# Optimization experiments

Hardware: AMD Instinct MI355X
Metric: run time of the kernel (lower is better)

## Reference

```python
import jax, jax.numpy as jnp
import numpy as np

B, N, C, H, D, K = 4, 8192, 384, 12, 2, 256
M = N // K          # 32 members per cluster
CH = C // H         # 32 head dim


def setup_inputs() -> dict:
    key = jax.random.key(0)
    ks = jax.random.split(key, 8)
    pos = jax.random.uniform(ks[0], (B, N, D), jnp.float32) * 100.0
    feat = jax.random.normal(ks[1], (B, N, C), jnp.float32)
    # each batch's points partitioned into K clusters of M members (a permutation)
    perms = jax.vmap(lambda kk: jax.random.permutation(kk, N))(jax.random.split(ks[2], B))
    member_idx = perms.reshape(B * K, M).astype(jnp.int32)               # z x m
    batch_idx = jnp.broadcast_to(
        jnp.repeat(jnp.arange(B, dtype=jnp.int32), K)[:, None], (B * K, M))
    w = 0.02
    qkv_w = jax.random.normal(ks[3], (3 * C, C), jnp.float32) * w
    qkv_b = jnp.zeros((3 * C,), jnp.float32)
    pos_w = jax.random.normal(ks[4], (H, D), jnp.float32) * w
    pos_b = jnp.zeros((H,), jnp.float32)
    proj_w = jax.random.normal(ks[5], (C, C), jnp.float32) * w
    proj_b = jnp.zeros((C,), jnp.float32)
    return dict(pos=pos, feat=feat, member_idx=member_idx, batch_idx=batch_idx,
                qkv_w=qkv_w, qkv_b=qkv_b, pos_w=pos_w, pos_b=pos_b,
                proj_w=proj_w, proj_b=proj_b, k=K)


def reference(pos, feat, member_idx, batch_idx, qkv_w, qkv_b, pos_w, pos_b,
              proj_w, proj_b, k):
    # attend_means=True, mask=None, cluster_score=None, q_subsample_idx=None path
    b, n, c = feat.shape
    d = pos.shape[2]
    h = pos_w.shape[0]
    ch = c // h
    z, m = member_idx.shape
    scale = ch ** -0.5

    qkv = feat @ qkv_w.T + qkv_b            # b,n,3c
    q = qkv[..., :c]                        # b,n,c
    kv = qkv[..., c:]                       # b,n,2c

    pos_orig = pos
    pos_n = pos / jnp.max(pos.reshape(-1, d), axis=0)   # per-coordinate max norm

    # irregular gather of kv / pos per cluster member
    kv_g = kv[batch_idx, member_idx]        # z,m,2c
    pos_g = pos_n[batch_idx, member_idx]    # z,m,d

    # cluster_score=None, mask=None -> uniform weights 1/m (mean over members)
    kv_mean = jnp.mean(kv_g, axis=1).reshape(b, k, 2, h, ch)
    pos_mean = jnp.mean(pos_g, axis=1).reshape(b, k, d)

    key_ = kv_mean[:, :, 0].transpose(0, 2, 1, 3)   # b,h,k,ch
    v = kv_mean[:, :, 1].transpose(0, 2, 1, 3)      # b,h,k,ch
    qh = q.reshape(b, n, h, ch).transpose(0, 2, 1, 3) * scale  # b,h,n,ch

    attn = jnp.einsum('bhnc,bhkc->bhnk', qh, key_)  # b,h,n,k
    rel_pos = pos_mean[:, None, :, :] - pos_orig[:, :, None, :]  # b,n,k,d
    pos_bias = jnp.einsum('bnkd,hd->bhnk', rel_pos, pos_w) + pos_b[None, :, None, None]
    attn = jax.nn.softmax(attn + pos_bias, axis=-1)

    out = jnp.einsum('bhnk,bhkc->bnhc', attn, v).reshape(b, n, c)
    return out @ proj_w.T + proj_b
```

## Files before the change

### kernel.cpp

```cpp
#include <hip/hip_runtime.h>

typedef __attribute__((ext_vector_type(8))) short bf16x8;
typedef __attribute__((ext_vector_type(4))) float f32x4;

#define MFMA16(a,b,c) __builtin_amdgcn_mfma_f32_16x16x32_bf16((a),(b),(c),0,0,0)

__device__ __forceinline__ float b2f(unsigned short u){
  union { unsigned u; float f; } x; x.u = ((unsigned)u) << 16; return x.f;
}
__device__ __forceinline__ unsigned short f2b(float f){
  union { float f; unsigned u; } x; x.f = f;
  unsigned r = x.u + 0x7FFFu + ((x.u >> 16) & 1u);
  return (unsigned short)(r >> 16);
}
__device__ __forceinline__ unsigned pk_rne(float a, float b){
  unsigned ua = __float_as_uint(a), ub = __float_as_uint(b);
  ua += 0x7FFFu + ((ua >> 16) & 1u);
  ub += 0x7FFFu + ((ub >> 16) & 1u);
  return __builtin_amdgcn_perm(ub, ua, 0x07060302u);
}
__device__ __forceinline__ unsigned pk_trunc(float a, float b){
  return __builtin_amdgcn_perm(__float_as_uint(b), __float_as_uint(a), 0x07060302u);
}
__device__ __forceinline__ bf16x8 mk8(unsigned a, unsigned b, unsigned c, unsigned d){
  union { uint4 u; bf16x8 h; } x; x.u = make_uint4(a,b,c,d); return x.h;
}
__device__ __forceinline__ int permp(int cl){
  return (cl & 0xE0) | (((cl >> 2) & 3) << 3) | (((cl >> 4) & 1) << 2) | (cl & 3);
}

typedef __attribute__((address_space(3))) unsigned int lds_u32;
typedef const __attribute__((address_space(1))) unsigned int glb_u32;
__device__ __forceinline__ void gl_lds16(const void* g, void* l){
  __builtin_amdgcn_global_load_lds((glb_u32*)g, (lds_u32*)l, 16, 0, 0);
}

__global__ __launch_bounds__(256) void prep_kernel(
    const float* __restrict__ pos, unsigned* __restrict__ pmax,
    const float* __restrict__ qkv_w, unsigned short* __restrict__ qkvwb,
    const float* __restrict__ proj_w, unsigned short* __restrict__ projwb)
{
  int bid = blockIdx.x, tid = threadIdx.x;
  if (bid < 64){
    int i = bid*256 + tid;
    float4 v = ((const float4*)pos)[i];
    float m0 = fmaxf(v.x, v.z), m1 = fmaxf(v.y, v.w);
    #pragma unroll
    for (int off = 32; off >= 1; off >>= 1){
      m0 = fmaxf(m0, __shfl_xor(m0, off, 64));
      m1 = fmaxf(m1, __shfl_xor(m1, off, 64));
    }
    if ((tid & 63) == 0){
      atomicMax(&pmax[0], __float_as_uint(m0));
      atomicMax(&pmax[1], __float_as_uint(m1));
    }
  } else {
    const float* in; unsigned short* o; long i;
    if (bid < 280){ in = qkv_w;  o = qkvwb;  i = (long)(bid-64)*256 + tid; }
    else          { in = proj_w; o = projwb; i = (long)(bid-280)*256 + tid; }
    const float4* p = (const float4*)(in + i*8);
    float4 a = p[0], b = p[1];
    *(uint4*)(o + i*8) = make_uint4(pk_rne(a.x,a.y), pk_rne(a.z,a.w),
                                    pk_rne(b.x,b.y), pk_rne(b.z,b.w));
  }
}

__global__ __launch_bounds__(192) void cluster_means_kernel(
    const float* __restrict__ feat, const float* __restrict__ pos,
    const int* __restrict__ member_idx, const int* __restrict__ batch_idx,
    unsigned short* __restrict__ fm, float* __restrict__ pm,
    unsigned short* __restrict__ featb)
{
  int t = threadIdx.x;
  int g = t / 96, tl = t - g*96;
  int z = blockIdx.x;
  __shared__ int bases[32];
  __shared__ float4 part[96];
  __shared__ float ppart[2];
  if (t < 32) bases[t] = batch_idx[z*32 + t]*8192 + member_idx[z*32 + t];
  __syncthreads();
  float4 a = {0.f,0.f,0.f,0.f};
  float p = 0.f;
  const float4* f4 = (const float4*)feat;
  #pragma unroll
  for (int mb = 0; mb < 2; mb++){
    float4 v[8]; int rows[8];
    #pragma unroll
    for (int m = 0; m < 8; m++){
      rows[m] = bases[g*16 + mb*8 + m];
      v[m] = f4[(long)rows[m]*96 + tl];
    }
    #pragma unroll
    for (int m = 0; m < 8; m++){
      *(uint2*)(featb + (long)rows[m]*384 + tl*4) =
          make_uint2(pk_rne(v[m].x, v[m].y), pk_rne(v[m].z, v[m].w));
      a.x += v[m].x; a.y += v[m].y; a.z += v[m].z; a.w += v[m].w;
      if (tl < 2) p += pos[(long)rows[m]*2 + tl];
    }
  }
  if (g == 1){ part[tl] = a; if (tl < 2) ppart[tl] = p; }
  __syncthreads();
  if (g == 0){
    float4 b = part[tl];
    a.x += b.x; a.y += b.y; a.z += b.z; a.w += b.w;
    unsigned d0 = pk_rne(a.x*(1.f/32.f), a.y*(1.f/32.f));
    unsigned d1 = pk_rne(a.z*(1.f/32.f), a.w*(1.f/32.f));
    *(uint2*)(fm + (long)z*384 + tl*4) = make_uint2(d0, d1);
    if (tl < 2) pm[z*2 + tl] = (p + ppart[tl]) * (1.f/32.f);
  }
}

__global__ __launch_bounds__(256) void bias_kernel(
    const float* __restrict__ pm, const float* __restrict__ pmaxf,
    const float* __restrict__ pos_w, const float* __restrict__ pos_b,
    unsigned short* __restrict__ wt)
{
  int idx = blockIdx.x*256 + threadIdx.x;
  int kc = idx & 255;
  int bh = idx >> 8;
  int h = bh % 12;
  float p0 = pm[((bh/12)*256 + kc)*2]   / pmaxf[0];
  float p1 = pm[((bh/12)*256 + kc)*2+1] / pmaxf[1];
  float bias = p0*pos_w[h*2] + p1*pos_w[h*2+1] + pos_b[h];
  wt[(bh << 8) + permp(kc)] = f2b(exp2f(bias * 1.44269504088896340f));
}

__global__ __launch_bounds__(256) void gemm_kv_kernel(
    const unsigned short* __restrict__ A, const unsigned short* __restrict__ W,
    const float* __restrict__ bias, unsigned short* __restrict__ kh,
    unsigned short* __restrict__ vt, const unsigned short* __restrict__ wt)
{
  __shared__ unsigned short As[64*64];
  __shared__ unsigned short Ws[128*64];
  const int N = 768, K = 384;
  int mt = blockIdx.x / 6, nt = blockIdx.x - mt*6;
  int m0 = mt << 6, n0 = nt << 7;
  int tid = threadIdx.x;
  int lane = tid & 63, wave = tid >> 6;
  int wr = (wave >> 1) << 5, wc = (wave & 1) << 6;
  int l15 = lane & 15, quad = lane >> 4;
  int sw = l15 & 7;
  int srow = tid >> 3, sc8 = tid & 7;

  f32x4 acc[2][4];
  #pragma unroll
  for (int i = 0; i < 2; i++)
    #pragma unroll
    for (int j = 0; j < 4; j++) acc[i][j] = (f32x4){0.f,0.f,0.f,0.f};

  for (int k0 = 0; k0 < K; k0 += 64){
    __syncthreads();
    #pragma unroll
    for (int it = 0; it < 2; it++){
      int r = srow + it*32;
      int gc8 = sc8 ^ (r & 7);
      gl_lds16(A + (long)(m0+r)*K + k0 + gc8*8, As + it*2048 + wave*512);
    }
    #pragma unroll
    for (int it = 0; it < 4; it++){
      int r = srow + it*32;
      int gc8 = sc8 ^ (r & 7);
      gl_lds16(W + (long)(n0+r)*K + k0 + gc8*8, Ws + it*2048 + wave*512);
    }
    __syncthreads();
    #pragma unroll
    for (int kk = 0; kk < 2; kk++){
      bf16x8 af[2], bfr[4];
      #pragma unroll
      for (int i = 0; i < 2; i++)
        af[i] = *(const bf16x8*)(As + (wr + i*16 + l15)*64 + (((kk<<2)+quad) ^ sw)*8);
      #pragma unroll
      for (int j = 0; j < 4; j++)
        bfr[j] = *(const bf16x8*)(Ws + (wc + j*16 + l15)*64 + (((kk<<2)+quad) ^ sw)*8);
      #pragma unroll
      for (int i = 0; i < 2; i++)
        #pragma unroll
        for (int j = 0; j < 4; j++)
          acc[i][j] = MFMA16(af[i], bfr[j], acc[i][j]);
    }
  }

  #pragma unroll
  for (int j = 0; j < 4; j++){
    int col = n0 + wc + j*16 + l15;
    float bv = bias[col];
    #pragma unroll
    for (int i = 0; i < 2; i++){
      int row0 = m0 + wr + i*16 + quad*4;
      #pragma unroll
      for (int r = 0; r < 4; r++){
        float v = acc[i][j][r] + bv;
        int row = row0 + r;
        int b = row >> 8, cl = row & 255;
        if (col < 384){
          int h = col >> 5, ch = col & 31;
          kh[((((long)b*12 + h)*256 + cl)*32) + ch] = f2b(v);
        } else {
          int cn = col - 384;
          int h = cn >> 5, ch = cn & 31;
          int pp = permp(cl);
          int c8 = (pp >> 3) ^ (ch & 7);
          float w = b2f(wt[(((long)b*12 + h) << 8) + pp]);
          vt[(((long)b*12 + h)*32 + ch)*256 + c8*8 + (pp & 7)] = f2b(v * w);
        }
      }
    }
  }
}

template<int OUT_F32, int AF32, int AHM, int CHM>
__global__ __launch_bounds__(512) void gemm_fn_kernel(
    const void* __restrict__ Av, const unsigned short* __restrict__ W,
    const float* __restrict__ bias, void* __restrict__ Cv, float out_scale)
{
  __shared__ unsigned short As[64*72];
  __shared__ unsigned short Ws[384*64];
  const int K = 384, N = 384;
  int m0 = blockIdx.x << 6;
  int tid = threadIdx.x;
  int lane = tid & 63, wave = tid >> 6;
  int l15 = lane & 15, quad = lane >> 4;
  int sw = l15 & 7;
  int srow = tid >> 3, sc8 = tid & 7;

  f32x4 acc[4][3];
  #pragma unroll
  for (int i = 0; i < 4; i++)
    #pragma unroll
    for (int j = 0; j < 3; j++) acc[i][j] = (f32x4){0.f,0.f,0.f,0.f};

  for (int k0 = 0; k0 < K; k0 += 64){
    __syncthreads();
    if (AF32){
      const float* Af = (const float*)Av;
      const float4* src = (const float4*)(Af + (long)(m0+srow)*K + k0 + sc8*8);
      float4 v0 = src[0], v1 = src[1];
      *(uint4*)(As + srow*72 + sc8*8) = make_uint4(pk_rne(v0.x,v0.y), pk_rne(v0.z,v0.w),
                                                   pk_rne(v1.x,v1.y), pk_rne(v1.z,v1.w));
    } else {
      const unsigned short* A = (const unsigned short*)Av;
      int gc8 = sc8 ^ (srow & 7);
      const unsigned short* src;
      if (AHM){
        int row = m0 + srow;
        int bb = row >> 13, tok = row & 8191;
        int ch = k0 + gc8*8;
        src = A + ((((long)(bb*12 + (ch >> 5))) << 13) + tok)*32 + (ch & 31);
      } else {
        src = A + (long)(m0+srow)*K + k0 + gc8*8;
      }
      gl_lds16(src, As + wave*512);
    }
    #pragma unroll
    for (int it = 0; it < 6; it++){
      int r = it*64 + srow;
      int gc8 = sc8 ^ (r & 7);
      gl_lds16(W + (long)r*K + k0 + gc8*8, Ws + it*4096 + wave*512);
    }
    __syncthreads();
    #pragma unroll
    for (int kk = 0; kk < 2; kk++){
      bf16x8 af[4];
      #pragma unroll
      for (int i = 0; i < 4; i++){
        int r = i*16 + l15;
        if (AF32) af[i] = *(const bf16x8*)(As + r*72 + ((kk<<2)+quad)*8);
        else      af[i] = *(const bf16x8*)(As + r*64 + (((kk<<2)+quad) ^ sw)*8);
      }
      #pragma unroll
      for (int j = 0; j < 3; j++){
        bf16x8 bfr = *(const bf16x8*)(Ws + (wave*48 + j*16 + l15)*64 + (((kk<<2)+quad) ^ sw)*8);
        #pragma unroll
        for (int i = 0; i < 4; i++)
          acc[i][j] = MFMA16(af[i], bfr, acc[i][j]);
      }
    }
  }

  #pragma unroll
  for (int j = 0; j < 3; j++){
    int col = wave*48 + j*16 + l15;
    float bv = bias[col];
    #pragma unroll
    for (int i = 0; i < 4; i++){
      int row0 = m0 + i*16 + quad*4;
      #pragma unroll
      for (int r = 0; r < 4; r++){
        float v = (acc[i][j][r] + bv) * out_scale;
        int row = row0 + r;
        if (OUT_F32){
          ((float*)Cv)[(long)row*N + col] = v;
        } else if (CHM){
          int bb = row >> 13, tok = row & 8191;
          ((unsigned short*)Cv)[((((long)(bb*12 + (col >> 5))) << 13) + tok)*32 + (col & 31)] = f2b(v);
        } else {
          ((unsigned short*)Cv)[(long)row*N + col] = f2b(v);
        }
      }
    }
  }
}

__global__ __launch_bounds__(256) void attn_kernel(
    const unsigned short* __restrict__ qhm,
    const unsigned short* __restrict__ kh,
    const unsigned short* __restrict__ vt,
    const unsigned short* __restrict__ wt,
    unsigned short* __restrict__ aohm)
{
  __shared__ unsigned short keyS[256*32];
  __shared__ unsigned short vTS[32*256];
  __shared__ unsigned short wS[256];

  int bid = blockIdx.x;
  int chunk = bid & 63;
  int bh = bid >> 6;
  int n0 = chunk << 7;
  int tid = threadIdx.x, lane = tid & 63, wave = tid >> 6;
  int l15 = lane & 15, quad = lane >> 4;
  int sw = l15 & 7;

  const unsigned short* khb = kh + (long)bh*8192;
  const unsigned short* vtb = vt + (long)bh*8192;
  #pragma unroll
  for (int it = 0; it < 4; it++){
    gl_lds16(khb + it*2048 + tid*8, keyS + it*2048 + wave*512);
    gl_lds16(vtb + it*2048 + tid*8, vTS  + it*2048 + wave*512);
  }
  if (tid < 32) *(uint4*)(wS + tid*8) = *(const uint4*)(wt + ((long)bh << 8) + tid*8);

  long qbase = ((long)bh*8192 + n0 + wave*32 + l15)*32 + quad*8;
  bf16x8 aq0 = *(const bf16x8*)(qhm + qbase);
  bf16x8 aq1 = *(const bf16x8*)(qhm + qbase + 512);
  __syncthreads();

  f32x4 o00 = {0.f,0.f,0.f,0.f}, o01 = {0.f,0.f,0.f,0.f}, os0 = {0.f,0.f,0.f,0.f};
  f32x4 o10 = {0.f,0.f,0.f,0.f}, o11 = {0.f,0.f,0.f,0.f}, os1 = {0.f,0.f,0.f,0.f};
  #pragma unroll
  for (int ks = 0; ks < 8; ks++){
    bf16x8 bk0 = *(const bf16x8*)(keyS + ((2*ks  )*16 + l15)*32 + quad*8);
    bf16x8 bk1 = *(const bf16x8*)(keyS + ((2*ks+1)*16 + l15)*32 + quad*8);
    f32x4 z4 = {0.f,0.f,0.f,0.f};
    f32x4 s00 = MFMA16(bk0, aq0, z4);
    f32x4 s01 = MFMA16(bk1, aq0, z4);
    f32x4 s10 = MFMA16(bk0, aq1, z4);
    f32x4 s11 = MFMA16(bk1, aq1, z4);
    #pragma unroll
    for (int c = 0; c < 4; c++){
      s00[c] = exp2f(s00[c]); s01[c] = exp2f(s01[c]);
      s10[c] = exp2f(s10[c]); s11[c] = exp2f(s11[c]);
    }
    bf16x8 pf0 = mk8(pk_trunc(s00[0],s00[1]), pk_trunc(s00[2],s00[3]),
                     pk_trunc(s01[0],s01[1]), pk_trunc(s01[2],s01[3]));
    bf16x8 pf1 = mk8(pk_trunc(s10[0],s10[1]), pk_trunc(s10[2],s10[3]),
                     pk_trunc(s11[0],s11[1]), pk_trunc(s11[2],s11[3]));
    int c8 = (4*ks + quad) ^ sw;
    bf16x8 a0 = *(const bf16x8*)(vTS + l15*256      + c8*8);
    bf16x8 a1 = *(const bf16x8*)(vTS + (16+l15)*256 + c8*8);
    bf16x8 wf = *(const bf16x8*)(wS + ks*32 + quad*8);
    o00 = MFMA16(a0, pf0, o00);
    o01 = MFMA16(a1, pf0, o01);
    os0 = MFMA16(wf, pf0, os0);
    o10 = MFMA16(a0, pf1, o10);
    o11 = MFMA16(a1, pf1, o11);
    os1 = MFMA16(wf, pf1, os1);
  }

  float inv0 = 1.f / os0[0];
  float inv1 = 1.f / os1[0];
  long ob0 = ((long)bh*8192 + n0 + wave*32 + l15)*32 + quad*4;
  *(uint2*)(aohm + ob0)      = make_uint2(pk_rne(o00[0]*inv0, o00[1]*inv0),
                                          pk_rne(o00[2]*inv0, o00[3]*inv0));
  *(uint2*)(aohm + ob0 + 16) = make_uint2(pk_rne(o01[0]*inv0, o01[1]*inv0),
                                          pk_rne(o01[2]*inv0, o01[3]*inv0));
  long ob1 = ob0 + 512;
  *(uint2*)(aohm + ob1)      = make_uint2(pk_rne(o10[0]*inv1, o10[1]*inv1),
                                          pk_rne(o10[2]*inv1, o10[3]*inv1));
  *(uint2*)(aohm + ob1 + 16) = make_uint2(pk_rne(o11[0]*inv1, o11[1]*inv1),
                                          pk_rne(o11[2]*inv1, o11[3]*inv1));
}

extern "C" void kernel_launch(void* const* d_in, const int* in_sizes, int n_in,
                              void* d_out, int out_size, void* d_ws, size_t ws_size,
                              hipStream_t stream)
{
  const float* pos      = (const float*)d_in[0];
  const float* feat     = (const float*)d_in[1];
  const int* member_idx = (const int*)d_in[2];
  const int* batch_idx  = (const int*)d_in[3];
  const float* qkv_w    = (const float*)d_in[4];
  const float* qkv_b    = (const float*)d_in[5];
  const float* pos_w    = (const float*)d_in[6];
  const float* pos_b    = (const float*)d_in[7];
  const float* proj_w   = (const float*)d_in[8];
  const float* proj_b   = (const float*)d_in[9];
  float* out = (float*)d_out;

  char* ws = (char*)d_ws;
  float* pmax           = (float*)ws;
  float* pm             = (float*)(ws + 256);
  unsigned short* fm    = (unsigned short*)(ws + 8704);
  unsigned short* kh    = (unsigned short*)(ws + 795136);
  unsigned short* vt    = (unsigned short*)(ws + 1581568);
  unsigned short* wt    = (unsigned short*)(ws + 2368000);
  unsigned short* q_s   = (unsigned short*)(ws + 2417152);
  unsigned short* ao    = (unsigned short*)(ws + 27582976);
  unsigned short* qkvwb = (unsigned short*)(ws + 52748800);
  unsigned short* projwb= (unsigned short*)(ws + 53633536);
  unsigned short* featb = (unsigned short*)(ws + 53928448);

  hipMemsetAsync(pmax, 0, 8, stream);
  prep_kernel<<<352, 256, 0, stream>>>(pos, (unsigned*)pmax, qkv_w, qkvwb, proj_w, projwb);
  cluster_means_kernel<<<1024, 192, 0, stream>>>(feat, pos, member_idx, batch_idx, fm, pm, featb);
  bias_kernel<<<48, 256, 0, stream>>>(pm, pmax, pos_w, pos_b, wt);
  gemm_kv_kernel<<<96, 256, 0, stream>>>(fm, qkvwb + 384*384, qkv_b + 384, kh, vt, wt);
  gemm_fn_kernel<0,0,0,1><<<512, 512, 0, stream>>>(featb, qkvwb, qkv_b, q_s,
                                                   0.17677669529663687f * 1.44269504088896340f);
  attn_kernel<<<3072, 256, 0, stream>>>(q_s, kh, vt, wt, ao);
  gemm_fn_kernel<1,0,1,0><<<512, 512, 0, stream>>>(ao, projwb, proj_b, out, 1.0f);
}
```

Before: 206.1 us.

## Double-buffer GEMM LDS staging and merge prep with cluster-means kernel

Fuses the weight conversion, position-max reduction and cluster-means gather into one launch, and computes the cluster position sums with a wave shuffle. The GEMM k-loop now double-buffers its A and W LDS tiles so the next tile's global-to-LDS loads overlap the current MFMAs, with one barrier per step. It also drops the fp32-A path. The doubled LDS footprint (about 112 KB) limits occupancy, and correctness relies on async LDS loads completing before the barrier.

```diff
diff --git a/kernel.cpp b/kernel.cpp
--- a/kernel.cpp
+++ b/kernel.cpp
@@ -35,78 +35,79 @@
   __builtin_amdgcn_global_load_lds((glb_u32*)g, (lds_u32*)l, 16, 0, 0);
 }
 
-__global__ __launch_bounds__(256) void prep_kernel(
+__global__ __launch_bounds__(192) void prep_means_kernel(
     const float* __restrict__ pos, unsigned* __restrict__ pmax,
     const float* __restrict__ qkv_w, unsigned short* __restrict__ qkvwb,
-    const float* __restrict__ proj_w, unsigned short* __restrict__ projwb)
-{
-  int bid = blockIdx.x, tid = threadIdx.x;
-  if (bid < 64){
-    int i = bid*256 + tid;
-    float4 v = ((const float4*)pos)[i];
-    float m0 = fmaxf(v.x, v.z), m1 = fmaxf(v.y, v.w);
-    #pragma unroll
-    for (int off = 32; off >= 1; off >>= 1){
-      m0 = fmaxf(m0, __shfl_xor(m0, off, 64));
-      m1 = fmaxf(m1, __shfl_xor(m1, off, 64));
-    }
-    if ((tid & 63) == 0){
-      atomicMax(&pmax[0], __float_as_uint(m0));
-      atomicMax(&pmax[1], __float_as_uint(m1));
-    }
-  } else {
+    const float* __restrict__ proj_w, unsigned short* __restrict__ projwb,
+    const float* __restrict__ feat,
+    const int* __restrict__ member_idx, const int* __restrict__ batch_idx,
+    unsigned short* __restrict__ fm, float* __restrict__ pm,
+    unsigned short* __restrict__ featb)
+{
+  int bid = blockIdx.x, t = threadIdx.x;
+  if (bid < 1024){
+    int g = t / 96, tl = t - g*96;
+    int z = bid;
+    __shared__ int bases[32];
+    __shared__ float4 part[96];
+    if (t < 32) bases[t] = batch_idx[z*32 + t]*8192 + member_idx[z*32 + t];
+    __syncthreads();
+    if (t < 32){
+      float2 pp = ((const float2*)pos)[bases[t]];
+      #pragma unroll
+      for (int off = 16; off >= 1; off >>= 1){
+        pp.x += __shfl_xor(pp.x, off, 32);
+        pp.y += __shfl_xor(pp.y, off, 32);
+      }
+      if (t == 0){ pm[z*2] = pp.x*(1.f/32.f); pm[z*2+1] = pp.y*(1.f/32.f); }
+    }
+    float4 v[16]; int rows[16];
+    const float4* f4 = (const float4*)feat;
+    #pragma unroll
+    for (int m = 0; m < 16; m++){
+      rows[m] = bases[g*16 + m];
+      v[m] = f4[(long)rows[m]*96 + tl];
+    }
+    float4 a = {0.f,0.f,0.f,0.f};
+    #pragma unroll
+    for (int m = 0; m < 16; m++){
+      *(uint2*)(featb + (long)rows[m]*384 + tl*4) =
+          make_uint2(pk_rne(v[m].x, v[m].y), pk_rne(v[m].z, v[m].w));
+      a.x += v[m].x; a.y += v[m].y; a.z += v[m].z; a.w += v[m].w;
+    }
+    if (g == 1) part[tl] = a;
+    __syncthreads();
+    if (g == 0){
+      float4 b = part[tl];
+      a.x += b.x; a.y += b.y; a.z += b.z; a.w += b.w;
+      unsigned d0 = pk_rne(a.x*(1.f/32.f), a.y*(1.f/32.f));
+      unsigned d1 = pk_rne(a.z*(1.f/32.f), a.w*(1.f/32.f));
+      *(uint2*)(fm + (long)z*384 + tl*4) = make_uint2(d0, d1);
+    }
+  } else if (bid < 1408){
+    int u = (bid - 1024)*192 + t;
     const float* in; unsigned short* o; long i;
-    if (bid < 280){ in = qkv_w;  o = qkvwb;  i = (long)(bid-64)*256 + tid; }
-    else          { in = proj_w; o = projwb; i = (long)(bid-280)*256 + tid; }
+    if (u < 55296){ in = qkv_w;  o = qkvwb;  i = u; }
+    else          { in = proj_w; o = projwb; i = u - 55296; }
     const float4* p = (const float4*)(in + i*8);
     float4 a = p[0], b = p[1];
     *(uint4*)(o + i*8) = make_uint4(pk_rne(a.x,a.y), pk_rne(a.z,a.w),
                                     pk_rne(b.x,b.y), pk_rne(b.z,b.w));
-  }
-}
-
-__global__ __launch_bounds__(192) void cluster_means_kernel(
-    const float* __restrict__ feat, const float* __restrict__ pos,
-    const int* __restrict__ member_idx, const int* __restrict__ batch_idx,
-    unsigned short* __restrict__ fm, float* __restrict__ pm,
-    unsigned short* __restrict__ featb)
-{
-  int t = threadIdx.x;
-  int g = t / 96, tl = t - g*96;
-  int z = blockIdx.x;
-  __shared__ int bases[32];
-  __shared__ float4 part[96];
-  __shared__ float ppart[2];
-  if (t < 32) bases[t] = batch_idx[z*32 + t]*8192 + member_idx[z*32 + t];
-  __syncthreads();
-  float4 a = {0.f,0.f,0.f,0.f};
-  float p = 0.f;
-  const float4* f4 = (const float4*)feat;
-  #pragma unroll
-  for (int mb = 0; mb < 2; mb++){
-    float4 v[8]; int rows[8];
-    #pragma unroll
-    for (int m = 0; m < 8; m++){
-      rows[m] = bases[g*16 + mb*8 + m];
-      v[m] = f4[(long)rows[m]*96 + tl];
-    }
-    #pragma unroll
-    for (int m = 0; m < 8; m++){
-      *(uint2*)(featb + (long)rows[m]*384 + tl*4) =
-          make_uint2(pk_rne(v[m].x, v[m].y), pk_rne(v[m].z, v[m].w));
-      a.x += v[m].x; a.y += v[m].y; a.z += v[m].z; a.w += v[m].w;
-      if (tl < 2) p += pos[(long)rows[m]*2 + tl];
-    }
-  }
-  if (g == 1){ part[tl] = a; if (tl < 2) ppart[tl] = p; }
-  __syncthreads();
-  if (g == 0){
-    float4 b = part[tl];
-    a.x += b.x; a.y += b.y; a.z += b.z; a.w += b.w;
-    unsigned d0 = pk_rne(a.x*(1.f/32.f), a.y*(1.f/32.f));
-    unsigned d1 = pk_rne(a.z*(1.f/32.f), a.w*(1.f/32.f));
-    *(uint2*)(fm + (long)z*384 + tl*4) = make_uint2(d0, d1);
-    if (tl < 2) pm[z*2 + tl] = (p + ppart[tl]) * (1.f/32.f);
+  } else {
+    int i = (bid - 1408)*192 + t;
+    if (i < 16384){
+      float4 v = ((const float4*)pos)[i];
+      float m0 = fmaxf(v.x, v.z), m1 = fmaxf(v.y, v.w);
+      #pragma unroll
+      for (int off = 32; off >= 1; off >>= 1){
+        m0 = fmaxf(m0, __shfl_xor(m0, off, 64));
+        m1 = fmaxf(m1, __shfl_xor(m1, off, 64));
+      }
+      if ((t & 63) == 0){
+        atomicMax(&pmax[0], __float_as_uint(m0));
+        atomicMax(&pmax[1], __float_as_uint(m1));
+      }
+    }
   }
 }
 
@@ -208,13 +209,13 @@
   }
 }
 
-template<int OUT_F32, int AF32, int AHM, int CHM>
+template<int OUT_F32, int AHM, int CHM>
 __global__ __launch_bounds__(512) void gemm_fn_kernel(
-    const void* __restrict__ Av, const unsigned short* __restrict__ W,
+    const unsigned short* __restrict__ A, const unsigned short* __restrict__ W,
     const float* __restrict__ bias, void* __restrict__ Cv, float out_scale)
 {
-  __shared__ unsigned short As[64*72];
-  __shared__ unsigned short Ws[384*64];
+  __shared__ unsigned short As[2][64*64];
+  __shared__ unsigned short Ws[2][384*64];
   const int K = 384, N = 384;
   int m0 = blockIdx.x << 6;
   int tid = threadIdx.x;
@@ -229,52 +230,47 @@
     #pragma unroll
     for (int j = 0; j < 3; j++) acc[i][j] = (f32x4){0.f,0.f,0.f,0.f};
 
-  for (int k0 = 0; k0 < K; k0 += 64){
-    __syncthreads();
-    if (AF32){
-      const float* Af = (const float*)Av;
-      const float4* src = (const float4*)(Af + (long)(m0+srow)*K + k0 + sc8*8);
-      float4 v0 = src[0], v1 = src[1];
-      *(uint4*)(As + srow*72 + sc8*8) = make_uint4(pk_rne(v0.x,v0.y), pk_rne(v0.z,v0.w),
-                                                   pk_rne(v1.x,v1.y), pk_rne(v1.z,v1.w));
+  auto stage = [&](int buf, int k0){
+    int gc8 = sc8 ^ (srow & 7);
+    const unsigned short* asrc;
+    if (AHM){
+      int row = m0 + srow;
+      int bb = row >> 13, tok = row & 8191;
+      int ch = k0 + gc8*8;
+      asrc = A + ((((long)(bb*12 + (ch >> 5))) << 13) + tok)*32 + (ch & 31);
     } else {
-      const unsigned short* A = (const unsigned short*)Av;
-      int gc8 = sc8 ^ (srow & 7);
-      const unsigned short* src;
-      if (AHM){
-        int row = m0 + srow;
-        int bb = row >> 13, tok = row & 8191;
-        int ch = k0 + gc8*8;
-        src = A + ((((long)(bb*12 + (ch >> 5))) << 13) + tok)*32 + (ch & 31);
-      } else {
-        src = A + (long)(m0+srow)*K + k0 + gc8*8;
-      }
-      gl_lds16(src, As + wave*512);
-    }
+      asrc = A + (long)(m0+srow)*K + k0 + gc8*8;
+    }
+    gl_lds16(asrc, &As[buf][wave*512]);
     #pragma unroll
     for (int it = 0; it < 6; it++){
       int r = it*64 + srow;
-      int gc8 = sc8 ^ (r & 7);
-      gl_lds16(W + (long)r*K + k0 + gc8*8, Ws + it*4096 + wave*512);
-    }
-    __syncthreads();
+      int g2 = sc8 ^ (r & 7);
+      gl_lds16(W + (long)r*K + k0 + g2*8, &Ws[buf][it*4096 + wave*512]);
+    }
+  };
+
+  stage(0, 0);
+  __syncthreads();
+  #pragma unroll
+  for (int t = 0; t < 6; t++){
+    if (t < 5) stage((t+1)&1, (t+1)*64);
+    int cur = t & 1;
     #pragma unroll
     for (int kk = 0; kk < 2; kk++){
       bf16x8 af[4];
       #pragma unroll
-      for (int i = 0; i < 4; i++){
-        int r = i*16 + l15;
-        if (AF32) af[i] = *(const bf16x8*)(As + r*72 + ((kk<<2)+quad)*8);
-        else      af[i] = *(const bf16x8*)(As + r*64 + (((kk<<2)+quad) ^ sw)*8);
-      }
+      for (int i = 0; i < 4; i++)
+        af[i] = *(const bf16x8*)(&As[cur][(i*16 + l15)*64 + (((kk<<2)+quad) ^ sw)*8]);
       #pragma unroll
       for (int j = 0; j < 3; j++){
-        bf16x8 bfr = *(const bf16x8*)(Ws + (wave*48 + j*16 + l15)*64 + (((kk<<2)+quad) ^ sw)*8);
+        bf16x8 bfr = *(const bf16x8*)(&Ws[cur][(wave*48 + j*16 + l15)*64 + (((kk<<2)+quad) ^ sw)*8]);
         #pragma unroll
         for (int i = 0; i < 4; i++)
           acc[i][j] = MFMA16(af[i], bfr, acc[i][j]);
       }
     }
+    __syncthreads();
   }
 
   #pragma unroll
@@ -410,12 +406,13 @@
   unsigned short* featb = (unsigned short*)(ws + 53928448);
 
   hipMemsetAsync(pmax, 0, 8, stream);
-  prep_kernel<<<352, 256, 0, stream>>>(pos, (unsigned*)pmax, qkv_w, qkvwb, proj_w, projwb);
-  cluster_means_kernel<<<1024, 192, 0, stream>>>(feat, pos, member_idx, batch_idx, fm, pm, featb);
+  prep_means_kernel<<<1494, 192, 0, stream>>>(pos, (unsigned*)pmax, qkv_w, qkvwb,
+                                              proj_w, projwb, feat, member_idx,
+                                              batch_idx, fm, pm, featb);
   bias_kernel<<<48, 256, 0, stream>>>(pm, pmax, pos_w, pos_b, wt);
   gemm_kv_kernel<<<96, 256, 0, stream>>>(fm, qkvwb + 384*384, qkv_b + 384, kh, vt, wt);
-  gemm_fn_kernel<0,0,0,1><<<512, 512, 0, stream>>>(featb, qkvwb, qkv_b, q_s,
-                                                   0.17677669529663687f * 1.44269504088896340f);
+  gemm_fn_kernel<0,0,1><<<512, 512, 0, stream>>>(featb, qkvwb, qkv_b, q_s,
+                                                 0.17677669529663687f * 1.44269504088896340f);
   attn_kernel<<<3072, 256, 0, stream>>>(q_s, kh, vt, wt, ao);
-  gemm_fn_kernel<1,0,1,0><<<512, 512, 0, stream>>>(ao, projwb, proj_b, out, 1.0f);
-}
+  gemm_fn_kernel<1,1,0><<<512, 512, 0, stream>>>(ao, projwb, proj_b, out, 1.0f);
+}
```

After: 211.4 us. 2.5% more time.
